# Performance work log

Measured on AMD Instinct MI355X. Metric: run time of the kernel, lower is better.

Reference implementation:

```python
import jax, jax.numpy as jnp
import numpy as np

EPS = 1e-6
THRESHOLD = 0.99
MAX_STEPS = 4
MIN_STEPS = 1
N_HEAD = 8
B, N, D, V, L, F, RCF = 1, 256, 512, 32000, 2, 1536, 2048


def rmsnorm(x, w):
    return x * jax.lax.rsqrt(jnp.mean(x * x, axis=-1, keepdims=True) + EPS) * w


def rope(x, base=10000.0):
    # x: [B, N, H, hd] -> rotary embedding (rotate-half convention)
    n, hd = x.shape[1], x.shape[-1]
    half = hd // 2
    inv = 1.0 / (base ** (jnp.arange(half, dtype=jnp.float32) * 2.0 / hd))
    ang = jnp.arange(n, dtype=jnp.float32)[:, None] * inv[None, :]  # [N, half]
    cos = jnp.cos(ang)[None, :, None, :]
    sin = jnp.sin(ang)[None, :, None, :]
    x1, x2 = x[..., :half], x[..., half:]
    return jnp.concatenate([x1 * cos - x2 * sin, x1 * sin + x2 * cos], axis=-1)


def attention(x, wqkv, wo):
    b, n, d = x.shape
    hd = d // N_HEAD
    q, k, v = jnp.split(x @ wqkv, 3, axis=-1)
    q = rope(q.reshape(b, n, N_HEAD, hd))
    k = rope(k.reshape(b, n, N_HEAD, hd))
    v = v.reshape(b, n, N_HEAD, hd)
    scores = jnp.einsum('bqhd,bkhd->bhqk', q, k) / np.float32(np.sqrt(hd))
    causal = jnp.tril(jnp.ones((n, n), dtype=bool))
    scores = jnp.where(causal, scores, jnp.float32(-1e30))
    a = jax.nn.softmax(scores, axis=-1)
    out = jnp.einsum('bhqk,bkhd->bqhd', a, v).reshape(b, n, d)
    return out @ wo


def backbone(input_ids, emb, attn_norm_w, mlp_norm_w, wqkv, wo, w_gate, w_up, w_down, final_norm_w):
    x = emb[input_ids]  # [B, N, D]
    for l in range(L):  # small fixed layer count
        x = x + attention(rmsnorm(x, attn_norm_w[l]), wqkv[l], wo[l])
        h = rmsnorm(x, mlp_norm_w[l])
        x = x + (jax.nn.silu(h @ w_gate[l]) * (h @ w_up[l])) @ w_down[l]  # SwiGLU
    return rmsnorm(x, final_norm_w)


def refinement_step(states, rc_norm_w, rc_w1, rc_w2, w_y, w_delta, w_halt, b_halt):
    h = rmsnorm(states, rc_norm_w)
    y_logits = h @ w_y                                   # [B, N, V]
    refined = states + jax.nn.gelu(h @ rc_w1) @ rc_w2    # [B, N, D]
    delta_logits = rmsnorm(refined, rc_norm_w) @ w_delta # [B, N, V]
    halt = jax.nn.sigmoid(h @ w_halt + b_halt)           # [B, N]
    combined = y_logits + delta_logits                   # compute_prediction
    return combined, halt, refined


def act_combine(halt_probs, step_logits):
    # Vectorized version of the per-(b,n) ACT halting loop.
    # halt_probs: [B, N, S]; step_logits: [B, N, S, V]
    p = halt_probs.at[..., :MIN_STEPS].set(0.0)  # min-step masking (max_steps > min_steps)
    cum = jnp.cumsum(p, axis=-1)
    prev = cum - p                      # exclusive cumulative halting prob
    running = prev < THRESHOLD          # step still executes
    is_last = jnp.arange(p.shape[-1]) == p.shape[-1] - 1
    use_rem = running & ((cum >= THRESHOLD) | is_last)  # halting step gets remainder
    weights = jnp.where(running, jnp.where(use_rem, 1.0 - prev, p), 0.0)
    final = jnp.einsum('bns,bnsv->bnv', weights, step_logits)
    remainder = jnp.sum(jnp.where(use_rem, 1.0 - prev, 0.0), axis=-1)
    ponder = jnp.sum(running, axis=-1).astype(p.dtype) + remainder  # N + R ponder cost
    return final, ponder, weights


def reference(input_ids, emb, attn_norm_w, mlp_norm_w, wqkv, wo, w_gate, w_up, w_down,
              final_norm_w, rc_norm_w, rc_w1, rc_w2, w_y, w_delta, w_halt, b_halt):
    hidden = backbone(input_ids, emb, attn_norm_w, mlp_norm_w, wqkv, wo,
                      w_gate, w_up, w_down, final_norm_w)
    states = hidden
    logits_steps, halt_steps = [], []
    for _ in range(MAX_STEPS):  # fixed refinement unroll
        combined, halt, states = refinement_step(states, rc_norm_w, rc_w1, rc_w2,
                                                 w_y, w_delta, w_halt, b_halt)
        logits_steps.append(combined)
        halt_steps.append(halt)
    step_logits = jnp.stack(logits_steps, axis=2)  # [B, N, S, V]
    halt_probs = jnp.stack(halt_steps, axis=2)     # [B, N, S]
    final_logits, ponder_costs, all_weights = act_combine(halt_probs, step_logits)
    return final_logits, ponder_costs, all_weights


def setup_inputs() -> dict:
    key = jax.random.key(0)
    ks = jax.random.split(key, 16)
    s = 0.02
    return {
        'input_ids': jax.random.randint(ks[0], (B, N), 0, V),
        'emb': jax.random.normal(ks[1], (V, D), jnp.float32) * s,
        'attn_norm_w': jnp.ones((L, D), jnp.float32),
        'mlp_norm_w': jnp.ones((L, D), jnp.float32),
        'wqkv': jax.random.normal(ks[2], (L, D, 3 * D), jnp.float32) * s,
        'wo': jax.random.normal(ks[3], (L, D, D), jnp.float32) * s,
        'w_gate': jax.random.normal(ks[4], (L, D, F), jnp.float32) * s,
        'w_up': jax.random.normal(ks[5], (L, D, F), jnp.float32) * s,
        'w_down': jax.random.normal(ks[6], (L, F, D), jnp.float32) * s,
        'final_norm_w': jnp.ones((D,), jnp.float32),
        'rc_norm_w': jnp.ones((D,), jnp.float32),
        'rc_w1': jax.random.normal(ks[7], (D, RCF), jnp.float32) * s,
        'rc_w2': jax.random.normal(ks[8], (RCF, D), jnp.float32) * s,
        'w_y': jax.random.normal(ks[9], (D, V), jnp.float32) * s,
        'w_delta': jax.random.normal(ks[10], (D, V), jnp.float32) * s,
        'w_halt': jax.random.normal(ks[11], (D,), jnp.float32) * s,
        'b_halt': jnp.zeros((), jnp.float32),
    }
```

## Files before the change

kernel.cpp:

```cpp
#include <hip/hip_runtime.h>
#include <hip/hip_bf16.h>

#define NTOK   256
#define DMODEL 512
#define NHEAD  8
#define HD     64
#define HALF   32
#define FF     1536
#define RCFF   2048
#define VOCAB  32000
#define NLAYER 2
#define NSTEPS 4
#define EPSV   1e-6f
#define THR    0.99f

typedef __attribute__((ext_vector_type(8))) short bf16x8;
typedef __attribute__((ext_vector_type(4))) float f32x4;
typedef __attribute__((ext_vector_type(16))) float f32x16;

__device__ __forceinline__ short f2b(float x) {
    return (short)__hip_bfloat16_raw(__float2bfloat16(x)).x;
}

__global__ __launch_bounds__(256) void k_embed_norm(const int* __restrict__ ids,
                                                    const float* __restrict__ emb,
                                                    const float* __restrict__ w,
                                                    float* __restrict__ x,
                                                    float* __restrict__ xn) {
    int row = blockIdx.x, t = threadIdx.x;
    int id = ids[row];
    const float* er = emb + (size_t)id * DMODEL;
    float v0 = er[t], v1 = er[t + 256];
    float ss = v0 * v0 + v1 * v1;
    __shared__ float red[4];
    int lane = t & 63, wv = t >> 6;
    for (int o = 32; o > 0; o >>= 1) ss += __shfl_xor(ss, o);
    if (lane == 0) red[wv] = ss;
    __syncthreads();
    float tot = red[0] + red[1] + red[2] + red[3];
    float scale = rsqrtf(tot * (1.f / DMODEL) + EPSV);
    size_t base = (size_t)row * DMODEL;
    x[base + t] = v0;
    x[base + t + 256] = v1;
    xn[base + t] = v0 * scale * w[t];
    xn[base + t + 256] = v1 * scale * w[t + 256];
}

__global__ __launch_bounds__(256) void k_rmsnorm(const float* __restrict__ in,
                                                 const float* __restrict__ w,
                                                 float* __restrict__ out) {
    int row = blockIdx.x;
    const float* xr = in + (size_t)row * DMODEL;
    float s = 0.f;
    for (int d = threadIdx.x; d < DMODEL; d += 256) { float v = xr[d]; s += v * v; }
    __shared__ float red[4];
    int lane = threadIdx.x & 63, wv = threadIdx.x >> 6;
    for (int o = 32; o > 0; o >>= 1) s += __shfl_xor(s, o);
    if (lane == 0) red[wv] = s;
    __syncthreads();
    float tot = red[0] + red[1] + red[2] + red[3];
    float scale = rsqrtf(tot * (1.f / DMODEL) + EPSV);
    for (int d = threadIdx.x; d < DMODEL; d += 256)
        out[(size_t)row * DMODEL + d] = xr[d] * scale * w[d];
}

__global__ __launch_bounds__(256) void k_mm_part(const float* __restrict__ A,
                                                 const float* __restrict__ W,
                                                 float* __restrict__ Cp,
                                                 int K, int N, int kc) {
    __shared__ float As[16][68];
    __shared__ float Ws[16][68];
    const int bn = blockIdx.x * 64;
    const int bm = blockIdx.y * 64;
    const int kz = blockIdx.z * kc;
    const int tx = threadIdx.x & 15;
    const int ty = threadIdx.x >> 4;
    float ar[4], wr[4];
#pragma unroll
    for (int r = 0; r < 4; ++r) {
        int idx = threadIdx.x + r * 256;
        int m = idx >> 4, kk = idx & 15;
        ar[r] = A[(size_t)(bm + m) * K + kz + kk];
        int n = idx & 63, kw = idx >> 6;
        wr[r] = W[(size_t)(kz + kw) * N + bn + n];
    }
    float acc[4][4] = {};
    for (int k0 = kz; k0 < kz + kc; k0 += 16) {
#pragma unroll
        for (int r = 0; r < 4; ++r) {
            int idx = threadIdx.x + r * 256;
            int m = idx >> 4, kk = idx & 15;
            As[kk][m] = ar[r];
            int n = idx & 63, kw = idx >> 6;
            Ws[kw][n] = wr[r];
        }
        __syncthreads();
        if (k0 + 16 < kz + kc) {
#pragma unroll
            for (int r = 0; r < 4; ++r) {
                int idx = threadIdx.x + r * 256;
                int m = idx >> 4, kk = idx & 15;
                ar[r] = A[(size_t)(bm + m) * K + k0 + 16 + kk];
                int n = idx & 63, kw = idx >> 6;
                wr[r] = W[(size_t)(k0 + 16 + kw) * N + bn + n];
            }
        }
#pragma unroll
        for (int kk = 0; kk < 16; ++kk) {
            float4 av = *(const float4*)&As[kk][ty * 4];
            float4 bv = *(const float4*)&Ws[kk][tx * 4];
            float a[4] = {av.x, av.y, av.z, av.w};
            float b[4] = {bv.x, bv.y, bv.z, bv.w};
#pragma unroll
            for (int i = 0; i < 4; ++i)
#pragma unroll
                for (int j = 0; j < 4; ++j)
                    acc[i][j] = fmaf(a[i], b[j], acc[i][j]);
        }
        __syncthreads();
    }
    float* cp = Cp + (size_t)blockIdx.z * (size_t)(gridDim.y * 64) * N;
#pragma unroll
    for (int i = 0; i < 4; ++i) {
        int m = bm + ty * 4 + i;
#pragma unroll
        for (int j = 0; j < 4; ++j)
            cp[(size_t)m * N + bn + tx * 4 + j] = acc[i][j];
    }
}

__global__ __launch_bounds__(256) void k_gu_part(const float* __restrict__ A,
                                                 const float* __restrict__ Wg,
                                                 const float* __restrict__ Wu,
                                                 float* __restrict__ GU) {
    __shared__ float As[16][68];
    __shared__ float Ws[16][68];
    const int bn = blockIdx.x * 64;
    const int bm = blockIdx.y * 64;
    const int z = blockIdx.z;
    const float* W = (z >> 1) ? Wu : Wg;
    const int kz = (z & 1) * 256;
    const int tx = threadIdx.x & 15;
    const int ty = threadIdx.x >> 4;
    float ar[4], wr[4];
#pragma unroll
    for (int r = 0; r < 4; ++r) {
        int idx = threadIdx.x + r * 256;
        int m = idx >> 4, kk = idx & 15;
        ar[r] = A[(size_t)(bm + m) * DMODEL + kz + kk];
        int n = idx & 63, kw = idx >> 6;
        wr[r] = W[(size_t)(kz + kw) * FF + bn + n];
    }
    float acc[4][4] = {};
    for (int k0 = kz; k0 < kz + 256; k0 += 16) {
#pragma unroll
        for (int r = 0; r < 4; ++r) {
            int idx = threadIdx.x + r * 256;
            int m = idx >> 4, kk = idx & 15;
            As[kk][m] = ar[r];
            int n = idx & 63, kw = idx >> 6;
            Ws[kw][n] = wr[r];
        }
        __syncthreads();
        if (k0 + 16 < kz + 256) {
#pragma unroll
            for (int r = 0; r < 4; ++r) {
                int idx = threadIdx.x + r * 256;
                int m = idx >> 4, kk = idx & 15;
                ar[r] = A[(size_t)(bm + m) * DMODEL + k0 + 16 + kk];
                int n = idx & 63, kw = idx >> 6;
                wr[r] = W[(size_t)(k0 + 16 + kw) * FF + bn + n];
            }
        }
#pragma unroll
        for (int kk = 0; kk < 16; ++kk) {
            float4 av = *(const float4*)&As[kk][ty * 4];
            float4 bv = *(const float4*)&Ws[kk][tx * 4];
            float a[4] = {av.x, av.y, av.z, av.w};
            float b[4] = {bv.x, bv.y, bv.z, bv.w};
#pragma unroll
            for (int i = 0; i < 4; ++i)
#pragma unroll
                for (int j = 0; j < 4; ++j)
                    acc[i][j] = fmaf(a[i], b[j], acc[i][j]);
        }
        __syncthreads();
    }
    float* cp = GU + (size_t)z * (NTOK * FF);
#pragma unroll
    for (int i = 0; i < 4; ++i) {
        int m = bm + ty * 4 + i;
#pragma unroll
        for (int j = 0; j < 4; ++j)
            cp[(size_t)m * FF + bn + tx * 4 + j] = acc[i][j];
    }
}

__global__ void k_mm_finish(const float* __restrict__ Cp, const float* __restrict__ res,
                            float* __restrict__ C, int tot, int zstride, int nz, int act) {
    int i = blockIdx.x * 256 + threadIdx.x;
    if (i >= tot) return;
    float s = 0.f;
    for (int z = 0; z < nz; ++z) s += Cp[(size_t)z * zstride + i];
    if (res) s += res[i];
    if (act == 1) {
        float xg = s;
        float inner = 0.79788456080286536f * (xg + 0.044715f * xg * xg * xg);
        s = 0.5f * xg * (1.f + tanhf(inner));
    }
    C[i] = s;
}

__global__ void k_finish_silumul(const float* __restrict__ GU, float* __restrict__ C) {
    int i = blockIdx.x * 256 + threadIdx.x;
    float g = GU[i] + GU[(size_t)(NTOK * FF) + i];
    float u = GU[(size_t)(2 * NTOK * FF) + i] + GU[(size_t)(3 * NTOK * FF) + i];
    float sig = 1.f / (1.f + expf(-g));
    C[i] = g * sig * u;
}

__global__ __launch_bounds__(256) void k_finish_norm(const float* __restrict__ Cp,
                                                     const float* __restrict__ res,
                                                     const float* __restrict__ normw,
                                                     float* __restrict__ out_raw,
                                                     float* __restrict__ out_norm,
                                                     int nz) {
    int row = blockIdx.x, t = threadIdx.x;
    int c0 = t, c1 = t + 256;
    size_t base = (size_t)row * DMODEL;
    float v0 = 0.f, v1 = 0.f;
    for (int z = 0; z < nz; ++z) {
        size_t zb = (size_t)z * (NTOK * DMODEL) + base;
        v0 += Cp[zb + c0];
        v1 += Cp[zb + c1];
    }
    v0 += res[base + c0];
    v1 += res[base + c1];
    float ss = v0 * v0 + v1 * v1;
    __shared__ float red[4];
    int lane = t & 63, wv = t >> 6;
    for (int o = 32; o > 0; o >>= 1) ss += __shfl_xor(ss, o);
    if (lane == 0) red[wv] = ss;
    __syncthreads();
    float tot = red[0] + red[1] + red[2] + red[3];
    float scale = rsqrtf(tot * (1.f / DMODEL) + EPSV);
    out_raw[base + c0] = v0;
    out_raw[base + c1] = v1;
    out_norm[base + c0] = v0 * scale * normw[c0];
    out_norm[base + c1] = v1 * scale * normw[c1];
}

__global__ __launch_bounds__(256) void k_qkv_finish_rope(const float* __restrict__ Cp,
                                                         float* __restrict__ qkv) {
    int pos = blockIdx.x, t = threadIdx.x;
    int h = t >> 5, d = t & 31;
    size_t base = (size_t)pos * FF;
    auto S = [&](int col) {
        float s = 0.f;
#pragma unroll
        for (int z = 0; z < 4; ++z) s += Cp[(size_t)z * (NTOK * FF) + base + col];
        return s;
    };
    int cq0 = h * HD + d, cq1 = cq0 + HALF;
    int ck0 = DMODEL + cq0, ck1 = ck0 + HALF;
    int cv0 = 2 * DMODEL + t, cv1 = cv0 + 256;
    float q0 = S(cq0), q1 = S(cq1);
    float k0 = S(ck0), k1 = S(ck1);
    float v0 = S(cv0), v1 = S(cv1);
    float inv = powf(10000.f, -(float)d / 32.f);
    float ang = (float)pos * inv;
    float c = cosf(ang), s = sinf(ang);
    qkv[base + cq0] = q0 * c - q1 * s;
    qkv[base + cq1] = q0 * s + q1 * c;
    qkv[base + ck0] = k0 * c - k1 * s;
    qkv[base + ck1] = k0 * s + k1 * c;
    qkv[base + cv0] = v0;
    qkv[base + cv1] = v1;
}

__global__ __launch_bounds__(256) void k_attn(const float* __restrict__ qkv,
                                              float* __restrict__ out) {
    int h = blockIdx.x;
    int qi = blockIdx.y;
    int t = threadIdx.x;
    __shared__ float qs[HD];
    __shared__ float ps[NTOK];
    __shared__ float red[4];
    __shared__ float red2[4];
    __shared__ float os[4][HD];
    if (t < HD) qs[t] = qkv[(size_t)qi * FF + h * HD + t];
    __syncthreads();
    float sc = -1e30f;
    if (t <= qi) {
        const float* kr = qkv + (size_t)t * FF + DMODEL + h * HD;
        float s = 0.f;
        for (int d = 0; d < HD; ++d) s = fmaf(qs[d], kr[d], s);
        sc = s * 0.125f;
    }
    float m = sc;
    for (int o = 32; o > 0; o >>= 1) m = fmaxf(m, __shfl_xor(m, o));
    int lane = t & 63, wv = t >> 6;
    if (lane == 0) red[wv] = m;
    __syncthreads();
    m = fmaxf(fmaxf(red[0], red[1]), fmaxf(red[2], red[3]));
    float e = (t <= qi) ? expf(sc - m) : 0.f;
    ps[t] = e;
    float sum = e;
    for (int o = 32; o > 0; o >>= 1) sum += __shfl_xor(sum, o);
    if (lane == 0) red2[wv] = sum;
    __syncthreads();
    sum = red2[0] + red2[1] + red2[2] + red2[3];
    float inv = 1.f / sum;
    int d = t & 63, g = t >> 6;
    float acc = 0.f;
    for (int ki = g; ki <= qi; ki += 4)
        acc = fmaf(ps[ki], qkv[(size_t)ki * FF + 2 * DMODEL + h * HD + d], acc);
    os[g][d] = acc * inv;
    __syncthreads();
    if (t < HD)
        out[(size_t)qi * DMODEL + h * HD + t] = os[0][t] + os[1][t] + os[2][t] + os[3][t];
}

__global__ __launch_bounds__(256) void k_haltactab(const float* __restrict__ H,
                                                   const float* __restrict__ wh,
                                                   const float* __restrict__ bptr,
                                                   float* __restrict__ ponder_out,
                                                   float* __restrict__ w_out,
                                                   __hip_bfloat16* __restrict__ A,
                                                   __hip_bfloat16* __restrict__ Bm) {
    int i = blockIdx.x, t = threadIdx.x;
    int lane = t & 63, wv = t >> 6;
    __shared__ float red[4];
    __shared__ float hvals[3];
    __shared__ float hw[4];
    for (int s = 1; s <= 3; ++s) {
        const float* hr = H + ((size_t)s * NTOK + i) * DMODEL;
        float a = hr[t] * wh[t] + hr[t + 256] * wh[t + 256];
        for (int o = 32; o > 0; o >>= 1) a += __shfl_xor(a, o);
        if (lane == 0) red[wv] = a;
        __syncthreads();
        if (t == 0)
            hvals[s - 1] = 1.f / (1.f + expf(-(red[0] + red[1] + red[2] + red[3] + bptr[0])));
        __syncthreads();
    }
    if (t == 0) {
        float p[4] = {0.f, hvals[0], hvals[1], hvals[2]};
        float cum = 0.f, rem = 0.f;
        int nrun = 0;
#pragma unroll
        for (int s = 0; s < 4; ++s) {
            float prev = cum;
            cum += p[s];
            bool running = prev < THR;
            bool use_rem = running && ((cum >= THR) || (s == 3));
            float v = 0.f;
            if (running) {
                v = use_rem ? (1.f - prev) : p[s];
                if (use_rem) rem += (1.f - prev);
                nrun++;
            }
            hw[s] = v;
            w_out[i * 4 + s] = v;
        }
        ponder_out[i] = (float)nrun + rem;
    }
    __syncthreads();
    float w0 = hw[0], w1 = hw[1], w2 = hw[2], w3 = hw[3];
    size_t base = (size_t)i * DMODEL;
#pragma unroll
    for (int r = 0; r < 2; ++r) {
        int d = t + r * 256;
        float h0 = H[base + d];
        float h1 = H[(size_t)(NTOK * DMODEL) + base + d];
        float h2 = H[(size_t)(2 * NTOK * DMODEL) + base + d];
        float h3 = H[(size_t)(3 * NTOK * DMODEL) + base + d];
        float h4 = H[(size_t)(4 * NTOK * DMODEL) + base + d];
        A[base + d]  = __float2bfloat16(w0 * h0 + w1 * h1 + w2 * h2 + w3 * h3);
        Bm[base + d] = __float2bfloat16(w0 * h1 + w1 * h2 + w2 * h3 + w3 * h4);
    }
}

__global__ __launch_bounds__(512) void k_logits_mfma(const __hip_bfloat16* __restrict__ Abf,
                                                     const __hip_bfloat16* __restrict__ Bbf,
                                                     const float* __restrict__ Wy,
                                                     const float* __restrict__ Wd,
                                                     float* __restrict__ out) {
    __shared__ short Alds[256 * 40];
    __shared__ short Blds[256 * 40];
    __shared__ short Wys[64 * 40];
    __shared__ short Wds[64 * 40];
    const int tid  = threadIdx.x;
    const int wave = tid >> 6;
    const int lane = tid & 63;
    const int l31  = lane & 31;
    const int hi8  = (lane >> 5) * 8;
    const int wv_row = (wave & 3) * 64;
    const int wv_col = (wave >> 2) * 32;

    const int sr0 = tid >> 2;
    const int skp = (tid & 3) * 8;
    const int wc  = tid & 63;
    const int wk4 = (tid >> 6) * 4;

    f32x16 acc0 = {};
    f32x16 acc1 = {};

    const size_t woff = (size_t)wk4 * VOCAB + blockIdx.x * 64 + wc;
    const float* gy = Wy + woff;
    const float* gd = Wd + woff;

    float rys[4], rds[4];
#pragma unroll
    for (int j = 0; j < 4; ++j) {
        rys[j] = gy[(size_t)j * VOCAB];
        rds[j] = gd[(size_t)j * VOCAB];
    }
    bf16x8 ra0 = *(const bf16x8*)(Abf + (size_t)sr0 * DMODEL + skp);
    bf16x8 ra1 = *(const bf16x8*)(Abf + (size_t)(sr0 + 128) * DMODEL + skp);
    bf16x8 rb0 = *(const bf16x8*)(Bbf + (size_t)sr0 * DMODEL + skp);
    bf16x8 rb1 = *(const bf16x8*)(Bbf + (size_t)(sr0 + 128) * DMODEL + skp);

    for (int t = 0; t < 16; ++t) {
        __syncthreads();
        {
            short4 sy, sd;
            sy.x = f2b(rys[0]); sy.y = f2b(rys[1]); sy.z = f2b(rys[2]); sy.w = f2b(rys[3]);
            sd.x = f2b(rds[0]); sd.y = f2b(rds[1]); sd.z = f2b(rds[2]); sd.w = f2b(rds[3]);
            *(short4*)&Wys[wc * 40 + wk4] = sy;
            *(short4*)&Wds[wc * 40 + wk4] = sd;
            *(bf16x8*)&Alds[sr0 * 40 + skp]         = ra0;
            *(bf16x8*)&Alds[(sr0 + 128) * 40 + skp] = ra1;
            *(bf16x8*)&Blds[sr0 * 40 + skp]         = rb0;
            *(bf16x8*)&Blds[(sr0 + 128) * 40 + skp] = rb1;
        }
        if (t < 15) {
            const int kn = (t + 1) * 32;
            const float* gy2 = gy + (size_t)kn * VOCAB;
            const float* gd2 = gd + (size_t)kn * VOCAB;
#pragma unroll
            for (int j = 0; j < 4; ++j) {
                rys[j] = gy2[(size_t)j * VOCAB];
                rds[j] = gd2[(size_t)j * VOCAB];
            }
            ra0 = *(const bf16x8*)(Abf + (size_t)sr0 * DMODEL + kn + skp);
            ra1 = *(const bf16x8*)(Abf + (size_t)(sr0 + 128) * DMODEL + kn + skp);
            rb0 = *(const bf16x8*)(Bbf + (size_t)sr0 * DMODEL + kn + skp);
            rb1 = *(const bf16x8*)(Bbf + (size_t)(sr0 + 128) * DMODEL + kn + skp);
        }
        __syncthreads();
#pragma unroll
        for (int h = 0; h < 2; ++h) {
            const int klo = h * 16 + hi8;
            const bf16x8 wyf = *(const bf16x8*)&Wys[(wv_col + l31) * 40 + klo];
            const bf16x8 wdf = *(const bf16x8*)&Wds[(wv_col + l31) * 40 + klo];
            const bf16x8 ay0 = *(const bf16x8*)&Alds[(wv_row + l31) * 40 + klo];
            const bf16x8 ay1 = *(const bf16x8*)&Alds[(wv_row + 32 + l31) * 40 + klo];
            const bf16x8 ad0 = *(const bf16x8*)&Blds[(wv_row + l31) * 40 + klo];
            const bf16x8 ad1 = *(const bf16x8*)&Blds[(wv_row + 32 + l31) * 40 + klo];
            acc0 = __builtin_amdgcn_mfma_f32_32x32x16_bf16(ay0, wyf, acc0, 0, 0, 0);
            acc0 = __builtin_amdgcn_mfma_f32_32x32x16_bf16(ad0, wdf, acc0, 0, 0, 0);
            acc1 = __builtin_amdgcn_mfma_f32_32x32x16_bf16(ay1, wyf, acc1, 0, 0, 0);
            acc1 = __builtin_amdgcn_mfma_f32_32x32x16_bf16(ad1, wdf, acc1, 0, 0, 0);
        }
    }
    const int col = blockIdx.x * 64 + wv_col + l31;
    const int rbase = (lane >> 5) * 4;
#pragma unroll
    for (int reg = 0; reg < 16; ++reg) {
        int rowin = (reg & 3) + 8 * (reg >> 2) + rbase;
        out[(size_t)(wv_row + rowin) * VOCAB + col] = acc0[reg];
        out[(size_t)(wv_row + 32 + rowin) * VOCAB + col] = acc1[reg];
    }
}

extern "C" void kernel_launch(void* const* d_in, const int* in_sizes, int n_in,
                              void* d_out, int out_size, void* d_ws, size_t ws_size,
                              hipStream_t stream) {
    const int*   ids          = (const int*)d_in[0];
    const float* emb          = (const float*)d_in[1];
    const float* attn_norm_w  = (const float*)d_in[2];
    const float* mlp_norm_w   = (const float*)d_in[3];
    const float* wqkv         = (const float*)d_in[4];
    const float* wo           = (const float*)d_in[5];
    const float* w_gate       = (const float*)d_in[6];
    const float* w_up         = (const float*)d_in[7];
    const float* w_down       = (const float*)d_in[8];
    const float* final_norm_w = (const float*)d_in[9];
    const float* rc_norm_w    = (const float*)d_in[10];
    const float* rc_w1        = (const float*)d_in[11];
    const float* rc_w2        = (const float*)d_in[12];
    const float* w_y          = (const float*)d_in[13];
    const float* w_delta      = (const float*)d_in[14];
    const float* w_halt       = (const float*)d_in[15];
    const float* b_halt       = (const float*)d_in[16];
    float* out = (float*)d_out;

    float* ws = (float*)d_ws;
    float* x       = ws + 0;
    float* xn      = ws + 131072;
    float* qkv     = ws + 262144;
    float* attnout = ws + 655360;
    float* g       = ws + 786432;
    float* t1      = ws + 1179648;
    float* states  = ws + 1703936;
    float* states2 = ws + 1835008;
    float* H       = ws + 1966080;
    __hip_bfloat16* Abf = (__hip_bfloat16*)(ws + 2623488);
    __hip_bfloat16* Bbf = (__hip_bfloat16*)(ws + 2754560);
    float* Cp      = ws + 2885632;
    float* GU      = ws + 1179648;

    k_embed_norm<<<NTOK, 256, 0, stream>>>(ids, emb, attn_norm_w, x, xn);
    for (int l = 0; l < NLAYER; ++l) {
        k_mm_part<<<dim3(FF / 64, 4, 4), 256, 0, stream>>>(
            xn, wqkv + (size_t)l * DMODEL * FF, Cp, DMODEL, FF, 128);
        k_qkv_finish_rope<<<NTOK, 256, 0, stream>>>(Cp, qkv);
        k_attn<<<dim3(NHEAD, NTOK), 256, 0, stream>>>(qkv, attnout);
        k_mm_part<<<dim3(DMODEL / 64, 4, 8), 256, 0, stream>>>(
            attnout, wo + (size_t)l * DMODEL * DMODEL, Cp, DMODEL, DMODEL, 64);
        k_finish_norm<<<NTOK, 256, 0, stream>>>(Cp, x, mlp_norm_w + l * DMODEL, x, xn, 8);
        k_gu_part<<<dim3(FF / 64, 4, 4), 256, 0, stream>>>(
            xn, w_gate + (size_t)l * DMODEL * FF, w_up + (size_t)l * DMODEL * FF, GU);
        k_finish_silumul<<<NTOK * FF / 256, 256, 0, stream>>>(GU, g);
        k_mm_part<<<dim3(DMODEL / 64, 4, 12), 256, 0, stream>>>(
            g, w_down + (size_t)l * FF * DMODEL, Cp, FF, DMODEL, 128);
        const float* nw = (l == 0) ? (attn_norm_w + DMODEL) : final_norm_w;
        float* nout = (l == 0) ? xn : states;
        k_finish_norm<<<NTOK, 256, 0, stream>>>(Cp, x, nw, x, nout, 12);
    }

    k_rmsnorm<<<NTOK, 256, 0, stream>>>(states, rc_norm_w, H);
    float* scur = states;
    float* snxt = states2;
    for (int s = 0; s < NSTEPS; ++s) {
        k_mm_part<<<dim3(RCFF / 64, 4, 4), 256, 0, stream>>>(
            H + (size_t)s * NTOK * DMODEL, rc_w1, Cp, DMODEL, RCFF, 128);
        k_mm_finish<<<NTOK * RCFF / 256, 256, 0, stream>>>(
            Cp, nullptr, t1, NTOK * RCFF, NTOK * RCFF, 4, 1);
        k_mm_part<<<dim3(DMODEL / 64, 4, 16), 256, 0, stream>>>(
            t1, rc_w2, Cp, RCFF, DMODEL, 128);
        k_finish_norm<<<NTOK, 256, 0, stream>>>(
            Cp, scur, rc_norm_w, snxt, H + (size_t)(s + 1) * NTOK * DMODEL, 16);
        float* tmp = scur; scur = snxt; snxt = tmp;
    }

    k_haltactab<<<NTOK, 256, 0, stream>>>(H, w_halt, b_halt,
                                          out + (size_t)NTOK * VOCAB,
                                          out + (size_t)NTOK * VOCAB + NTOK,
                                          Abf, Bbf);

    k_logits_mfma<<<VOCAB / 64, 512, 0, stream>>>(Abf, Bbf, w_y, w_delta, out);
}
```

Measured before the change: 372.2 us.

## Pre-convert vocab weights to tiled bf16 and stream them into MFMA registers

Adds a kernel that converts w_y and w_delta from fp32 into bf16 on every call and writes them in a per-tile, MFMA-fragment-ready layout in workspace. A new logits kernel then loads those weight fragments straight from global memory into registers, skipping the per-iteration fp32-to-bf16 conversion and the LDS staging of weights. The cost is an extra full pass over both large vocab matrices (fp32 read plus bf16 write) before the GEMM reads them again. The new path only runs when the workspace is large enough; otherwise the old kernel is kept.

```diff
diff --git a/kernel.cpp b/kernel.cpp
--- a/kernel.cpp
+++ b/kernel.cpp
@@ -13,6 +13,11 @@
 #define NSTEPS 4
 #define EPSV   1e-6f
 #define THR    0.99f
+
+#define NTILE     (VOCAB / 64)
+#define WT_MAT    (NTILE * DMODEL * 64)
+#define WT_OFF_F  5000000
+#define WS_NEED   ((size_t)(WT_OFF_F + 2 * WT_MAT / 2) * 4)
 
 typedef __attribute__((ext_vector_type(8))) short bf16x8;
 typedef __attribute__((ext_vector_type(4))) float f32x4;
@@ -380,6 +385,128 @@
     }
 }
 
+__global__ __launch_bounds__(256) void k_wconv(const float* __restrict__ Wy,
+                                               const float* __restrict__ Wd,
+                                               short* __restrict__ Wt) {
+    __shared__ short tl[4 * 2048];
+    const int t = threadIdx.x;
+    const int cb = blockIdx.x * 256;
+    const int kb = blockIdx.y * 32;
+    const int mat = blockIdx.z;
+    const float* W = mat ? Wd : Wy;
+#pragma unroll
+    for (int p = 0; p < 8; ++p) {
+        int row = kb + p * 4 + (t >> 6);
+        int col = cb + (t & 63) * 4;
+        float4 v = *(const float4*)&W[(size_t)row * VOCAB + col];
+        int ti = (t & 63) >> 4;
+        int ci = ((t & 63) * 4) & 63;
+        int ri = p * 4 + (t >> 6);
+        short4 s;
+        s.x = f2b(v.x); s.y = f2b(v.y); s.z = f2b(v.z); s.w = f2b(v.w);
+        *(short4*)&tl[ti * 2048 + ri * 64 + ci] = s;
+    }
+    __syncthreads();
+#pragma unroll
+    for (int ti = 0; ti < 4; ++ti) {
+        size_t doff = (size_t)mat * WT_MAT + (size_t)(cb / 64 + ti) * (DMODEL * 64)
+                    + (size_t)(kb / 8) * 512 + t * 8;
+        short v[8];
+#pragma unroll
+        for (int j = 0; j < 8; ++j)
+            v[j] = tl[ti * 2048 + ((t >> 6) * 8 + j) * 64 + (t & 63)];
+        *(bf16x8*)&Wt[doff] = *(bf16x8*)v;
+    }
+}
+
+__global__ __launch_bounds__(512) void k_logits_bf16t(const __hip_bfloat16* __restrict__ Abf,
+                                                      const __hip_bfloat16* __restrict__ Bbf,
+                                                      const short* __restrict__ Wt,
+                                                      float* __restrict__ out) {
+    __shared__ short Alds[256 * 40];
+    __shared__ short Blds[256 * 40];
+    const int tid  = threadIdx.x;
+    const int wave = tid >> 6;
+    const int lane = tid & 63;
+    const int l31  = lane & 31;
+    const int hi8  = (lane >> 5) * 8;
+    const int wv_row = (wave & 3) * 64;
+    const int wv_col = (wave >> 2) * 32;
+
+    const int sr0 = tid >> 2;
+    const int skp = (tid & 3) * 8;
+
+    f32x16 acc0 = {};
+    f32x16 acc1 = {};
+
+    const size_t wbase = (size_t)blockIdx.x * (DMODEL * 64)
+                       + (size_t)(wv_col + l31) * 8 + (size_t)(lane >> 5) * 512;
+    const short* wy = Wt + wbase;
+    const short* wd = Wt + (size_t)WT_MAT + wbase;
+
+    bf16x8 cwy0 = *(const bf16x8*)(wy);
+    bf16x8 cwy1 = *(const bf16x8*)(wy + 2 * 512);
+    bf16x8 cwd0 = *(const bf16x8*)(wd);
+    bf16x8 cwd1 = *(const bf16x8*)(wd + 2 * 512);
+    bf16x8 ra0 = *(const bf16x8*)(Abf + (size_t)sr0 * DMODEL + skp);
+    bf16x8 ra1 = *(const bf16x8*)(Abf + (size_t)(sr0 + 128) * DMODEL + skp);
+    bf16x8 rb0 = *(const bf16x8*)(Bbf + (size_t)sr0 * DMODEL + skp);
+    bf16x8 rb1 = *(const bf16x8*)(Bbf + (size_t)(sr0 + 128) * DMODEL + skp);
+
+    for (int t = 0; t < 16; ++t) {
+        __syncthreads();
+        *(bf16x8*)&Alds[sr0 * 40 + skp]         = ra0;
+        *(bf16x8*)&Alds[(sr0 + 128) * 40 + skp] = ra1;
+        *(bf16x8*)&Blds[sr0 * 40 + skp]         = rb0;
+        *(bf16x8*)&Blds[(sr0 + 128) * 40 + skp] = rb1;
+        bf16x8 nwy0, nwy1, nwd0, nwd1;
+        if (t < 15) {
+            const int kn = (t + 1) * 32;
+            const size_t kgoff = (size_t)(kn / 8) * 512;
+            nwy0 = *(const bf16x8*)(wy + kgoff);
+            nwy1 = *(const bf16x8*)(wy + kgoff + 2 * 512);
+            nwd0 = *(const bf16x8*)(wd + kgoff);
+            nwd1 = *(const bf16x8*)(wd + kgoff + 2 * 512);
+            ra0 = *(const bf16x8*)(Abf + (size_t)sr0 * DMODEL + kn + skp);
+            ra1 = *(const bf16x8*)(Abf + (size_t)(sr0 + 128) * DMODEL + kn + skp);
+            rb0 = *(const bf16x8*)(Bbf + (size_t)sr0 * DMODEL + kn + skp);
+            rb1 = *(const bf16x8*)(Bbf + (size_t)(sr0 + 128) * DMODEL + kn + skp);
+        }
+        __syncthreads();
+        {
+            const int klo = hi8;
+            const bf16x8 ay0 = *(const bf16x8*)&Alds[(wv_row + l31) * 40 + klo];
+            const bf16x8 ay1 = *(const bf16x8*)&Alds[(wv_row + 32 + l31) * 40 + klo];
+            const bf16x8 ad0 = *(const bf16x8*)&Blds[(wv_row + l31) * 40 + klo];
+            const bf16x8 ad1 = *(const bf16x8*)&Blds[(wv_row + 32 + l31) * 40 + klo];
+            acc0 = __builtin_amdgcn_mfma_f32_32x32x16_bf16(ay0, cwy0, acc0, 0, 0, 0);
+            acc0 = __builtin_amdgcn_mfma_f32_32x32x16_bf16(ad0, cwd0, acc0, 0, 0, 0);
+            acc1 = __builtin_amdgcn_mfma_f32_32x32x16_bf16(ay1, cwy0, acc1, 0, 0, 0);
+            acc1 = __builtin_amdgcn_mfma_f32_32x32x16_bf16(ad1, cwd0, acc1, 0, 0, 0);
+        }
+        {
+            const int klo = 16 + hi8;
+            const bf16x8 ay0 = *(const bf16x8*)&Alds[(wv_row + l31) * 40 + klo];
+            const bf16x8 ay1 = *(const bf16x8*)&Alds[(wv_row + 32 + l31) * 40 + klo];
+            const bf16x8 ad0 = *(const bf16x8*)&Blds[(wv_row + l31) * 40 + klo];
+            const bf16x8 ad1 = *(const bf16x8*)&Blds[(wv_row + 32 + l31) * 40 + klo];
+            acc0 = __builtin_amdgcn_mfma_f32_32x32x16_bf16(ay0, cwy1, acc0, 0, 0, 0);
+            acc0 = __builtin_amdgcn_mfma_f32_32x32x16_bf16(ad0, cwd1, acc0, 0, 0, 0);
+            acc1 = __builtin_amdgcn_mfma_f32_32x32x16_bf16(ay1, cwy1, acc1, 0, 0, 0);
+            acc1 = __builtin_amdgcn_mfma_f32_32x32x16_bf16(ad1, cwd1, acc1, 0, 0, 0);
+        }
+        cwy0 = nwy0; cwy1 = nwy1; cwd0 = nwd0; cwd1 = nwd1;
+    }
+    const int col = blockIdx.x * 64 + wv_col + l31;
+    const int rbase = (lane >> 5) * 4;
+#pragma unroll
+    for (int reg = 0; reg < 16; ++reg) {
+        int rowin = (reg & 3) + 8 * (reg >> 2) + rbase;
+        out[(size_t)(wv_row + rowin) * VOCAB + col] = acc0[reg];
+        out[(size_t)(wv_row + 32 + rowin) * VOCAB + col] = acc1[reg];
+    }
+}
+
 __global__ __launch_bounds__(512) void k_logits_mfma(const __hip_bfloat16* __restrict__ Abf,
                                                      const __hip_bfloat16* __restrict__ Bbf,
                                                      const float* __restrict__ Wy,
@@ -396,19 +523,15 @@
     const int hi8  = (lane >> 5) * 8;
     const int wv_row = (wave & 3) * 64;
     const int wv_col = (wave >> 2) * 32;
-
     const int sr0 = tid >> 2;
     const int skp = (tid & 3) * 8;
     const int wc  = tid & 63;
     const int wk4 = (tid >> 6) * 4;
-
     f32x16 acc0 = {};
     f32x16 acc1 = {};
-
     const size_t woff = (size_t)wk4 * VOCAB + blockIdx.x * 64 + wc;
     const float* gy = Wy + woff;
     const float* gd = Wd + woff;
-
     float rys[4], rds[4];
 #pragma unroll
     for (int j = 0; j < 4; ++j) {
@@ -419,7 +542,6 @@
     bf16x8 ra1 = *(const bf16x8*)(Abf + (size_t)(sr0 + 128) * DMODEL + skp);
     bf16x8 rb0 = *(const bf16x8*)(Bbf + (size_t)sr0 * DMODEL + skp);
     bf16x8 rb1 = *(const bf16x8*)(Bbf + (size_t)(sr0 + 128) * DMODEL + skp);
-
     for (int t = 0; t < 16; ++t) {
         __syncthreads();
         {
@@ -509,6 +631,11 @@
     __hip_bfloat16* Bbf = (__hip_bfloat16*)(ws + 2754560);
     float* Cp      = ws + 2885632;
     float* GU      = ws + 1179648;
+    short* Wt      = (short*)(ws + WT_OFF_F);
+    const bool use_bf16t = (ws_size >= WS_NEED);
+
+    if (use_bf16t)
+        k_wconv<<<dim3(VOCAB / 256, DMODEL / 32, 2), 256, 0, stream>>>(w_y, w_delta, Wt);
 
     k_embed_norm<<<NTOK, 256, 0, stream>>>(ids, emb, attn_norm_w, x, xn);
     for (int l = 0; l < NLAYER; ++l) {
@@ -549,5 +676,8 @@
                                           out + (size_t)NTOK * VOCAB + NTOK,
                                           Abf, Bbf);
 
-    k_logits_mfma<<<VOCAB / 64, 512, 0, stream>>>(Abf, Bbf, w_y, w_delta, out);
-}
+    if (use_bf16t)
+        k_logits_bf16t<<<NTILE, 512, 0, stream>>>(Abf, Bbf, Wt, out);
+    else
+        k_logits_mfma<<<NTILE, 512, 0, stream>>>(Abf, Bbf, w_y, w_delta, out);
+}
```

Result: slower. 398.8 us (+7.1%).
